# Performance work log

Hardware: AMD Instinct MI355X
Metric: run time of the kernel (lower is better)

## Reference

```python
import jax, jax.numpy as jnp
import numpy as np

LEAK = 0.95
EPS = 1e-4
THRESH = 1.0


def spike_fn(x):
    # forward of SurrogateBPFunction: heaviside(x > 0)
    return (x > 0).astype(x.dtype)


def setup_inputs() -> dict:
    key = jax.random.key(0)
    k1, k2, k3 = jax.random.split(key, 3)
    T, B, D_in, H, C = 20, 512, 4096, 1024, 100
    z = jax.random.normal(k1, (T, B, D_in), dtype=jnp.float32)
    # xavier_uniform with gain=2: bound = 2 * sqrt(6/(fan_in+fan_out))
    b1 = 2.0 * np.sqrt(6.0 / (D_in + H))
    W1 = jax.random.uniform(k2, (H, D_in), dtype=jnp.float32, minval=-b1, maxval=b1)
    b2 = 2.0 * np.sqrt(6.0 / (H + C))
    W2 = jax.random.uniform(k3, (C, H), dtype=jnp.float32, minval=-b2, maxval=b2)
    bn_gamma = jnp.ones((T, H), dtype=jnp.float32)
    return {"z": z, "W1": W1, "bn_gamma": bn_gamma, "W2": W2}


def reference(z, W1, bn_gamma, W2):
    T = z.shape[0]
    B = z.shape[1]
    H = W1.shape[0]
    C = W2.shape[0]

    def step(carry, xs):
        mem1, mem2 = carry
        inp_t, gamma = xs  # inp_t: [B, D_in], gamma: [H]
        h = jnp.einsum('bd,hd->bh', inp_t, W1)  # fc1, no bias
        # BatchNorm1d (training-mode batch stats, affine weight, no bias)
        mean = h.mean(axis=0)
        var = h.var(axis=0)  # biased variance, matches torch BN
        h = gamma * (h - mean) * jax.lax.rsqrt(var + EPS)
        mem1 = LEAK * mem1 + h
        mem_thr = mem1 / THRESH - 1.0
        out = spike_fn(mem_thr)
        rst = jnp.where(mem_thr > 0, THRESH, 0.0).astype(mem1.dtype)
        mem1 = mem1 - rst
        mem2 = mem2 + jnp.einsum('bh,ch->bc', out, W2)
        return (mem1, mem2), None

    mem1_0 = jnp.zeros((B, H), dtype=z.dtype)
    mem2_0 = jnp.zeros((B, C), dtype=z.dtype)
    (mem1, mem2), _ = jax.lax.scan(step, (mem1_0, mem2_0), (z, bn_gamma))
    return mem2 / T
```

## Files before the change

kernel.cpp:

```cpp
#include <hip/hip_runtime.h>
#include <hip/hip_bf16.h>
#include <stdint.h>

typedef _Float16 half8 __attribute__((ext_vector_type(8)));
typedef float f32x4 __attribute__((ext_vector_type(4)));

#define T_STEPS 20
#define B_SZ 512
#define D_IN 4096
#define H_SZ 1024
#define C_SZ 100
#define M_TOT (T_STEPS * B_SZ)
#define BK 32
#define KITERS (D_IN / BK)

__device__ __forceinline__ void gload16(const _Float16* g, _Float16* l) {
  __builtin_amdgcn_global_load_lds(
      (const __attribute__((address_space(1))) void*)g,
      (__attribute__((address_space(3))) void*)l, 16, 0, 0);
}

struct HL {
  half8 h;
  half8 l;
};
__device__ __forceinline__ HL split8(float4 a, float4 b) {
  HL r;
  auto p0 = __builtin_amdgcn_cvt_pkrtz(a.x, a.y);
  auto p1 = __builtin_amdgcn_cvt_pkrtz(a.z, a.w);
  auto p2 = __builtin_amdgcn_cvt_pkrtz(b.x, b.y);
  auto p3 = __builtin_amdgcn_cvt_pkrtz(b.z, b.w);
  r.h[0] = p0.x; r.h[1] = p0.y; r.h[2] = p1.x; r.h[3] = p1.y;
  r.h[4] = p2.x; r.h[5] = p2.y; r.h[6] = p3.x; r.h[7] = p3.y;
  auto q0 = __builtin_amdgcn_cvt_pkrtz(a.x - (float)p0.x, a.y - (float)p0.y);
  auto q1 = __builtin_amdgcn_cvt_pkrtz(a.z - (float)p1.x, a.w - (float)p1.y);
  auto q2 = __builtin_amdgcn_cvt_pkrtz(b.x - (float)p2.x, b.y - (float)p2.y);
  auto q3 = __builtin_amdgcn_cvt_pkrtz(b.z - (float)p3.x, b.w - (float)p3.y);
  r.l[0] = q0.x; r.l[1] = q0.y; r.l[2] = q1.x; r.l[3] = q1.y;
  r.l[4] = q2.x; r.l[5] = q2.y; r.l[6] = q3.x; r.l[7] = q3.y;
  return r;
}

__global__ void k_prep_frag(const float* __restrict__ Z, _Float16* __restrict__ Azh,
                            _Float16* __restrict__ Azl, const float* __restrict__ W1,
                            _Float16* __restrict__ Wfh, _Float16* __restrict__ Wfl) {
  const int ki = blockIdx.x;
  int rt = blockIdx.y;
  const float* src;
  _Float16 *dh, *dl;
  if (rt < 80) {
    src = Z; dh = Azh; dl = Azl;
  } else {
    rt -= 80; src = W1; dh = Wfh; dl = Wfl;
  }
  const int t = threadIdx.x;
#pragma unroll
  for (int p = 0; p < 2; ++p) {
    const int o = t + p * 256;
    const int fb = o >> 6;
    const int j = o & 63;
    const int q = j >> 4;
    const int r = j & 15;
    const float* s = src + (int64_t)(rt * 128 + fb * 16 + r) * D_IN + ki * 32 + q * 8;
    float4 a = *(const float4*)s;
    float4 b = *(const float4*)(s + 4);
    HL hl = split8(a, b);
    const int64_t d = (((int64_t)rt * 128 + ki) * 8 + fb) * 512 + j * 8;
    *(half8*)&dh[d] = hl.h;
    *(half8*)&dl[d] = hl.l;
  }
}

__global__ void k_prep_w2(const float* __restrict__ w2, _Float16* __restrict__ hi,
                          _Float16* __restrict__ lo) {
  int i = blockIdx.x * 256 + threadIdx.x;
  float v = (i < C_SZ * H_SZ) ? w2[i] : 0.0f;
  _Float16 h = (_Float16)v;
  hi[i] = h;
  lo[i] = (_Float16)(v - (float)h);
}

__global__ __launch_bounds__(256) void k_gemm1(
    const _Float16* __restrict__ Ahi, const _Float16* __restrict__ Alo,
    const _Float16* __restrict__ Whi, const _Float16* __restrict__ Wlo,
    float* __restrict__ Hbuf) {
  __shared__ _Float16 sAh[4096];
  __shared__ _Float16 sAl[4096];
  __shared__ _Float16 sWh[4096];
  __shared__ _Float16 sWl[4096];

  const int tid = threadIdx.x;
  const int lane = tid & 63;
  const int w = tid >> 6;

  const int bid = blockIdx.x;
  const int xcd = bid & 7;
  const int q = bid >> 3;
  const int mt = xcd * 10 + (q >> 3);
  const int nt = q & 7;

  const int ls = w * 512 + lane * 8;
  const _Float16* gAh = Ahi + (int64_t)mt * (128 * 4096) + ls;
  const _Float16* gAl = Alo + (int64_t)mt * (128 * 4096) + ls;
  const _Float16* gWh = Whi + (int64_t)nt * (128 * 4096) + ls;
  const _Float16* gWl = Wlo + (int64_t)nt * (128 * 4096) + ls;

  const int wm = (w >> 1) * 64;
  const int wn = (w & 1) * 64;
  const int ra = (wm >> 4) * 512 + lane * 8;
  const int rb = (wn >> 4) * 512 + lane * 8;
  const int fr = lane & 15;
  const int quad = lane >> 4;

  f32x4 acc[4][4] = {};

  for (int ki = 0; ki < KITERS; ++ki) {
    const int64_t so = (int64_t)ki * 4096;
    __syncthreads();
    gload16(gAh + so, &sAh[ls]);
    gload16(gAh + so + 2048, &sAh[ls + 2048]);
    gload16(gAl + so, &sAl[ls]);
    gload16(gAl + so + 2048, &sAl[ls + 2048]);
    gload16(gWh + so, &sWh[ls]);
    gload16(gWh + so + 2048, &sWh[ls + 2048]);
    gload16(gWl + so, &sWl[ls]);
    gload16(gWl + so + 2048, &sWl[ls + 2048]);
    __syncthreads();

    half8 ah[4], al[4], bh[4], bl[4];
#pragma unroll
    for (int i = 0; i < 4; ++i) {
      ah[i] = *(const half8*)&sAh[ra + i * 512];
      al[i] = *(const half8*)&sAl[ra + i * 512];
      bh[i] = *(const half8*)&sWh[rb + i * 512];
      bl[i] = *(const half8*)&sWl[rb + i * 512];
    }
#pragma unroll
    for (int a = 0; a < 4; ++a) {
#pragma unroll
      for (int b = 0; b < 4; ++b) {
        acc[a][b] = __builtin_amdgcn_mfma_f32_16x16x32_f16(ah[a], bh[b], acc[a][b], 0, 0, 0);
        acc[a][b] = __builtin_amdgcn_mfma_f32_16x16x32_f16(ah[a], bl[b], acc[a][b], 0, 0, 0);
        acc[a][b] = __builtin_amdgcn_mfma_f32_16x16x32_f16(al[a], bh[b], acc[a][b], 0, 0, 0);
      }
    }
  }

  const int64_t m0 = (int64_t)mt * 128;
  const int64_t n0 = (int64_t)nt * 128;
#pragma unroll
  for (int a = 0; a < 4; ++a) {
#pragma unroll
    for (int r = 0; r < 4; ++r) {
      const int64_t row = m0 + wm + a * 16 + quad * 4 + r;
      float* dst = Hbuf + row * H_SZ + n0 + wn + fr;
#pragma unroll
      for (int b = 0; b < 4; ++b) dst[b * 16] = acc[a][b][r];
    }
  }
}

__global__ void k_stats(const float* __restrict__ Hbuf, const float* __restrict__ gamma,
                        float* __restrict__ scale, float* __restrict__ shift) {
  const int t = blockIdx.y;
  const int tx = threadIdx.x & 63;
  const int ty = threadIdx.x >> 6;
  const int h = blockIdx.x * 64 + tx;
  const float* p = Hbuf + ((int64_t)t * B_SZ + ty * 128) * H_SZ + h;
  float s = 0.f, s2 = 0.f;
#pragma unroll 8
  for (int i = 0; i < 128; ++i) {
    float v = p[(int64_t)i * H_SZ];
    s += v;
    s2 += v * v;
  }
  __shared__ float ss[4][64];
  __shared__ float sq[4][64];
  ss[ty][tx] = s;
  sq[ty][tx] = s2;
  __syncthreads();
  if (ty == 0) {
    float a = ss[0][tx] + ss[1][tx] + ss[2][tx] + ss[3][tx];
    float b = sq[0][tx] + sq[1][tx] + sq[2][tx] + sq[3][tx];
    const float mean = a * (1.0f / B_SZ);
    const float var = b * (1.0f / B_SZ) - mean * mean;
    const float rs = rsqrtf(var + 1e-4f);
    const float sc = gamma[t * H_SZ + h] * rs;
    scale[t * H_SZ + h] = sc;
    shift[t * H_SZ + h] = -mean * sc;
  }
}

__global__ void k_recur(const float* __restrict__ Hbuf, const float* __restrict__ scale,
                        const float* __restrict__ shift, _Float16* __restrict__ S) {
  const int idx = blockIdx.x * 256 + threadIdx.x;
  const int b = idx >> 10;
  const int h = idx & 1023;
  float mem = 0.f;
  int cnt = 0;
#pragma unroll
  for (int t = 0; t < T_STEPS; ++t) {
    float v = Hbuf[((int64_t)(t * B_SZ + b) << 10) + h];
    v = v * scale[(t << 10) + h] + shift[(t << 10) + h];
    mem = 0.95f * mem + v;
    if (mem - 1.0f > 0.0f) {
      ++cnt;
      mem -= 1.0f;
    }
  }
  S[idx] = (_Float16)cnt;
}

__global__ void k_gemm2(const _Float16* __restrict__ S, const _Float16* __restrict__ W2h,
                        const _Float16* __restrict__ W2l, float* __restrict__ out) {
  const int wid = threadIdx.x >> 6;
  const int lane = threadIdx.x & 63;
  const int m0 = blockIdx.y * 64 + wid * 16;
  const int n0 = blockIdx.x * 16;
  const int fr = lane & 15;
  const int quad = lane >> 4;

  const _Float16* sp = S + (int64_t)(m0 + fr) * H_SZ + quad * 8;
  const _Float16* wph = W2h + (int64_t)(n0 + fr) * H_SZ + quad * 8;
  const _Float16* wpl = W2l + (int64_t)(n0 + fr) * H_SZ + quad * 8;

  f32x4 acc = {0.f, 0.f, 0.f, 0.f};
#pragma unroll 4
  for (int k = 0; k < H_SZ; k += 32) {
    half8 a = *(const half8*)(sp + k);
    half8 bh = *(const half8*)(wph + k);
    half8 bl = *(const half8*)(wpl + k);
    acc = __builtin_amdgcn_mfma_f32_16x16x32_f16(a, bh, acc, 0, 0, 0);
    acc = __builtin_amdgcn_mfma_f32_16x16x32_f16(a, bl, acc, 0, 0, 0);
  }
  const int col = n0 + fr;
  if (col < C_SZ) {
#pragma unroll
    for (int r = 0; r < 4; ++r) {
      const int row = m0 + quad * 4 + r;
      out[row * C_SZ + col] = acc[r] * (1.0f / T_STEPS);
    }
  }
}

extern "C" void kernel_launch(void* const* d_in, const int* in_sizes, int n_in,
                              void* d_out, int out_size, void* d_ws, size_t ws_size,
                              hipStream_t stream) {
  const float* z = (const float*)d_in[0];
  const float* W1 = (const float*)d_in[1];
  const float* gamma = (const float*)d_in[2];
  const float* W2 = (const float*)d_in[3];
  float* out = (float*)d_out;

  char* ws = (char*)d_ws;
  size_t off = 0;
  auto alloc = [&](size_t bytes) -> void* {
    void* p = ws + off;
    off += (bytes + 255) & ~(size_t)255;
    return p;
  };
  _Float16* Azh = (_Float16*)alloc((size_t)M_TOT * D_IN * 2);
  _Float16* Azl = (_Float16*)alloc((size_t)M_TOT * D_IN * 2);
  _Float16* Wfh = (_Float16*)alloc((size_t)H_SZ * D_IN * 2);
  _Float16* Wfl = (_Float16*)alloc((size_t)H_SZ * D_IN * 2);
  float* Hbuf = (float*)alloc((size_t)M_TOT * H_SZ * 4);
  float* scale = (float*)alloc((size_t)T_STEPS * H_SZ * 4);
  float* shift = (float*)alloc((size_t)T_STEPS * H_SZ * 4);
  _Float16* S = (_Float16*)alloc((size_t)B_SZ * H_SZ * 2);
  _Float16* W2h = (_Float16*)alloc((size_t)112 * H_SZ * 2);
  _Float16* W2l = (_Float16*)alloc((size_t)112 * H_SZ * 2);

  dim3 gp(KITERS, 88);
  k_prep_frag<<<gp, 256, 0, stream>>>(z, Azh, Azl, W1, Wfh, Wfl);
  k_prep_w2<<<(112 * H_SZ) / 256, 256, 0, stream>>>(W2, W2h, W2l);

  k_gemm1<<<640, 256, 0, stream>>>(Azh, Azl, Wfh, Wfl, Hbuf);

  dim3 gs(H_SZ / 64, T_STEPS);
  k_stats<<<gs, 256, 0, stream>>>(Hbuf, gamma, scale, shift);

  k_recur<<<(B_SZ * H_SZ) / 256, 256, 0, stream>>>(Hbuf, scale, shift, S);

  dim3 g2(7, 8);
  k_gemm2<<<g2, 256, 0, stream>>>(S, W2h, W2l, out);
}
```

Measured before the change: 548.9 us.

## Fuse BN stats into GEMM epilogue, merge prep kernels with LDS-staged transpose

Removes the separate BatchNorm statistics kernel. The GEMM1 epilogue now reduces per-column sum and sum of squares across lanes and adds them into global buffers with atomics, and the recurrence kernel derives mean and scale on the fly. The Z/W1 fragment prep kernel now reads full contiguous rows and restages them through padded LDS, and the W2 prep is folded into the same launch, cutting launches and improving read coalescing. The trade-offs are atomic contention, a memset, and redundant rsqrt work per element in the recurrence.

```diff
diff --git a/kernel.cpp b/kernel.cpp
--- a/kernel.cpp
+++ b/kernel.cpp
@@ -3,6 +3,7 @@
 #include <stdint.h>
 
 typedef _Float16 half8 __attribute__((ext_vector_type(8)));
+typedef _Float16 half4v __attribute__((ext_vector_type(4)));
 typedef float f32x4 __attribute__((ext_vector_type(4)));
 
 #define T_STEPS 20
@@ -14,38 +15,52 @@
 #define BK 32
 #define KITERS (D_IN / BK)
 
+#define PQ 136
+#define PKI 560
+
 __device__ __forceinline__ void gload16(const _Float16* g, _Float16* l) {
   __builtin_amdgcn_global_load_lds(
       (const __attribute__((address_space(1))) void*)g,
       (__attribute__((address_space(3))) void*)l, 16, 0, 0);
 }
 
-struct HL {
-  half8 h;
-  half8 l;
+struct HL4 {
+  half4v h;
+  half4v l;
 };
-__device__ __forceinline__ HL split8(float4 a, float4 b) {
-  HL r;
+__device__ __forceinline__ HL4 split4(float4 a) {
+  HL4 r;
   auto p0 = __builtin_amdgcn_cvt_pkrtz(a.x, a.y);
   auto p1 = __builtin_amdgcn_cvt_pkrtz(a.z, a.w);
-  auto p2 = __builtin_amdgcn_cvt_pkrtz(b.x, b.y);
-  auto p3 = __builtin_amdgcn_cvt_pkrtz(b.z, b.w);
-  r.h[0] = p0.x; r.h[1] = p0.y; r.h[2] = p1.x; r.h[3] = p1.y;
-  r.h[4] = p2.x; r.h[5] = p2.y; r.h[6] = p3.x; r.h[7] = p3.y;
+  r.h.x = p0.x; r.h.y = p0.y; r.h.z = p1.x; r.h.w = p1.y;
   auto q0 = __builtin_amdgcn_cvt_pkrtz(a.x - (float)p0.x, a.y - (float)p0.y);
   auto q1 = __builtin_amdgcn_cvt_pkrtz(a.z - (float)p1.x, a.w - (float)p1.y);
-  auto q2 = __builtin_amdgcn_cvt_pkrtz(b.x - (float)p2.x, b.y - (float)p2.y);
-  auto q3 = __builtin_amdgcn_cvt_pkrtz(b.z - (float)p3.x, b.w - (float)p3.y);
-  r.l[0] = q0.x; r.l[1] = q0.y; r.l[2] = q1.x; r.l[3] = q1.y;
-  r.l[4] = q2.x; r.l[5] = q2.y; r.l[6] = q3.x; r.l[7] = q3.y;
+  r.l.x = q0.x; r.l.y = q0.y; r.l.z = q1.x; r.l.w = q1.y;
   return r;
 }
 
-__global__ void k_prep_frag(const float* __restrict__ Z, _Float16* __restrict__ Azh,
-                            _Float16* __restrict__ Azl, const float* __restrict__ W1,
-                            _Float16* __restrict__ Wfh, _Float16* __restrict__ Wfl) {
-  const int ki = blockIdx.x;
-  int rt = blockIdx.y;
+__global__ __launch_bounds__(256) void k_prep(
+    const float* __restrict__ Z, _Float16* __restrict__ Azh, _Float16* __restrict__ Azl,
+    const float* __restrict__ W1, _Float16* __restrict__ Wfh, _Float16* __restrict__ Wfl,
+    const float* __restrict__ W2, _Float16* __restrict__ W2h, _Float16* __restrict__ W2l) {
+  const int bid = blockIdx.x;
+  const int tid = threadIdx.x;
+
+  if (bid >= 704) {
+    const int base = (bid - 704) * 1792;
+#pragma unroll
+    for (int i = 0; i < 7; ++i) {
+      const int idx = base + i * 256 + tid;
+      float v = (idx < C_SZ * H_SZ) ? W2[idx] : 0.0f;
+      _Float16 h = (_Float16)v;
+      W2h[idx] = h;
+      W2l[idx] = (_Float16)(v - (float)h);
+    }
+    return;
+  }
+
+  int rt = bid >> 3;
+  const int fb = bid & 7;
   const float* src;
   _Float16 *dh, *dl;
   if (rt < 80) {
@@ -53,37 +68,49 @@
   } else {
     rt -= 80; src = W1; dh = Wfh; dl = Wfl;
   }
-  const int t = threadIdx.x;
-#pragma unroll
-  for (int p = 0; p < 2; ++p) {
-    const int o = t + p * 256;
-    const int fb = o >> 6;
-    const int j = o & 63;
-    const int q = j >> 4;
-    const int r = j & 15;
-    const float* s = src + (int64_t)(rt * 128 + fb * 16 + r) * D_IN + ki * 32 + q * 8;
-    float4 a = *(const float4*)s;
-    float4 b = *(const float4*)(s + 4);
-    HL hl = split8(a, b);
-    const int64_t d = (((int64_t)rt * 128 + ki) * 8 + fb) * 512 + j * 8;
-    *(half8*)&dh[d] = hl.h;
-    *(half8*)&dl[d] = hl.l;
-  }
-}
-
-__global__ void k_prep_w2(const float* __restrict__ w2, _Float16* __restrict__ hi,
-                          _Float16* __restrict__ lo) {
-  int i = blockIdx.x * 256 + threadIdx.x;
-  float v = (i < C_SZ * H_SZ) ? w2[i] : 0.0f;
-  _Float16 h = (_Float16)v;
-  hi[i] = h;
-  lo[i] = (_Float16)(v - (float)h);
+  const float* rowbase = src + (int64_t)(rt * 128 + fb * 16) * D_IN;
+
+  __shared__ _Float16 sH[16 * PKI];
+  __shared__ _Float16 sL[16 * PKI];
+
+  for (int win = 0; win < 8; ++win) {
+#pragma unroll
+    for (int it = 0; it < 8; ++it) {
+      const int idx = it * 256 + tid;
+      const int r = idx >> 7;
+      const int c4 = idx & 127;
+      const int col = c4 * 4;
+      float4 v = *(const float4*)(rowbase + (int64_t)r * D_IN + win * 512 + col);
+      HL4 hl = split4(v);
+      const int ki_l = col >> 5;
+      const int q = (col >> 3) & 3;
+      const int k4 = col & 7;
+      const int d = ki_l * PKI + q * PQ + r * 8 + k4;
+      *(half4v*)&sH[d] = hl.h;
+      *(half4v*)&sL[d] = hl.l;
+    }
+    __syncthreads();
+#pragma unroll
+    for (int it = 0; it < 4; ++it) {
+      const int o = it * 256 + tid;
+      const int ki_l = o >> 6;
+      const int j = o & 63;
+      const int q = j >> 4;
+      const int r = j & 15;
+      const int sidx = ki_l * PKI + q * PQ + r * 8;
+      const int ki = win * 16 + ki_l;
+      const int64_t d = (((int64_t)rt * 128 + ki) * 8 + fb) * 512 + j * 8;
+      *(half8*)&dh[d] = *(const half8*)&sH[sidx];
+      *(half8*)&dl[d] = *(const half8*)&sL[sidx];
+    }
+    __syncthreads();
+  }
 }
 
 __global__ __launch_bounds__(256) void k_gemm1(
     const _Float16* __restrict__ Ahi, const _Float16* __restrict__ Alo,
     const _Float16* __restrict__ Whi, const _Float16* __restrict__ Wlo,
-    float* __restrict__ Hbuf) {
+    float* __restrict__ Hbuf, float* __restrict__ Ssum, float* __restrict__ Ssq) {
   __shared__ _Float16 sAh[4096];
   __shared__ _Float16 sAl[4096];
   __shared__ _Float16 sWh[4096];
@@ -158,41 +185,32 @@
       for (int b = 0; b < 4; ++b) dst[b * 16] = acc[a][b][r];
     }
   }
-}
-
-__global__ void k_stats(const float* __restrict__ Hbuf, const float* __restrict__ gamma,
-                        float* __restrict__ scale, float* __restrict__ shift) {
-  const int t = blockIdx.y;
-  const int tx = threadIdx.x & 63;
-  const int ty = threadIdx.x >> 6;
-  const int h = blockIdx.x * 64 + tx;
-  const float* p = Hbuf + ((int64_t)t * B_SZ + ty * 128) * H_SZ + h;
-  float s = 0.f, s2 = 0.f;
-#pragma unroll 8
-  for (int i = 0; i < 128; ++i) {
-    float v = p[(int64_t)i * H_SZ];
-    s += v;
-    s2 += v * v;
-  }
-  __shared__ float ss[4][64];
-  __shared__ float sq[4][64];
-  ss[ty][tx] = s;
-  sq[ty][tx] = s2;
-  __syncthreads();
-  if (ty == 0) {
-    float a = ss[0][tx] + ss[1][tx] + ss[2][tx] + ss[3][tx];
-    float b = sq[0][tx] + sq[1][tx] + sq[2][tx] + sq[3][tx];
-    const float mean = a * (1.0f / B_SZ);
-    const float var = b * (1.0f / B_SZ) - mean * mean;
-    const float rs = rsqrtf(var + 1e-4f);
-    const float sc = gamma[t * H_SZ + h] * rs;
-    scale[t * H_SZ + h] = sc;
-    shift[t * H_SZ + h] = -mean * sc;
-  }
-}
-
-__global__ void k_recur(const float* __restrict__ Hbuf, const float* __restrict__ scale,
-                        const float* __restrict__ shift, _Float16* __restrict__ S) {
+
+  const int t = mt >> 2;
+#pragma unroll
+  for (int b = 0; b < 4; ++b) {
+    float s = 0.f, s2 = 0.f;
+#pragma unroll
+    for (int a = 0; a < 4; ++a)
+#pragma unroll
+      for (int r = 0; r < 4; ++r) {
+        float v = acc[a][b][r];
+        s += v;
+        s2 += v * v;
+      }
+    s += __shfl_xor(s, 16);  s2 += __shfl_xor(s2, 16);
+    s += __shfl_xor(s, 32);  s2 += __shfl_xor(s2, 32);
+    if (quad == 0) {
+      const int h = (int)n0 + wn + fr + b * 16;
+      atomicAdd(&Ssum[t * H_SZ + h], s);
+      atomicAdd(&Ssq[t * H_SZ + h], s2);
+    }
+  }
+}
+
+__global__ void k_recur(const float* __restrict__ Hbuf, const float* __restrict__ Ssum,
+                        const float* __restrict__ Ssq, const float* __restrict__ gamma,
+                        _Float16* __restrict__ S) {
   const int idx = blockIdx.x * 256 + threadIdx.x;
   const int b = idx >> 10;
   const int h = idx & 1023;
@@ -200,8 +218,11 @@
   int cnt = 0;
 #pragma unroll
   for (int t = 0; t < T_STEPS; ++t) {
+    const float mean = Ssum[(t << 10) + h] * (1.0f / B_SZ);
+    const float var = Ssq[(t << 10) + h] * (1.0f / B_SZ) - mean * mean;
+    const float sc = gamma[(t << 10) + h] * rsqrtf(var + 1e-4f);
     float v = Hbuf[((int64_t)(t * B_SZ + b) << 10) + h];
-    v = v * scale[(t << 10) + h] + shift[(t << 10) + h];
+    v = (v - mean) * sc;
     mem = 0.95f * mem + v;
     if (mem - 1.0f > 0.0f) {
       ++cnt;
@@ -264,22 +285,19 @@
   _Float16* Wfh = (_Float16*)alloc((size_t)H_SZ * D_IN * 2);
   _Float16* Wfl = (_Float16*)alloc((size_t)H_SZ * D_IN * 2);
   float* Hbuf = (float*)alloc((size_t)M_TOT * H_SZ * 4);
-  float* scale = (float*)alloc((size_t)T_STEPS * H_SZ * 4);
-  float* shift = (float*)alloc((size_t)T_STEPS * H_SZ * 4);
+  float* Ssum = (float*)alloc((size_t)T_STEPS * H_SZ * 4);
+  float* Ssq = (float*)alloc((size_t)T_STEPS * H_SZ * 4);
   _Float16* S = (_Float16*)alloc((size_t)B_SZ * H_SZ * 2);
   _Float16* W2h = (_Float16*)alloc((size_t)112 * H_SZ * 2);
   _Float16* W2l = (_Float16*)alloc((size_t)112 * H_SZ * 2);
 
-  dim3 gp(KITERS, 88);
-  k_prep_frag<<<gp, 256, 0, stream>>>(z, Azh, Azl, W1, Wfh, Wfl);
-  k_prep_w2<<<(112 * H_SZ) / 256, 256, 0, stream>>>(W2, W2h, W2l);
-
-  k_gemm1<<<640, 256, 0, stream>>>(Azh, Azl, Wfh, Wfl, Hbuf);
-
-  dim3 gs(H_SZ / 64, T_STEPS);
-  k_stats<<<gs, 256, 0, stream>>>(Hbuf, gamma, scale, shift);
-
-  k_recur<<<(B_SZ * H_SZ) / 256, 256, 0, stream>>>(Hbuf, scale, shift, S);
+  hipMemsetAsync(Ssum, 0, (size_t)2 * T_STEPS * H_SZ * 4, stream);
+
+  k_prep<<<768, 256, 0, stream>>>(z, Azh, Azl, W1, Wfh, Wfl, W2, W2h, W2l);
+
+  k_gemm1<<<640, 256, 0, stream>>>(Azh, Azl, Wfh, Wfl, Hbuf, Ssum, Ssq);
+
+  k_recur<<<(B_SZ * H_SZ) / 256, 256, 0, stream>>>(Hbuf, Ssum, Ssq, gamma, S);
 
   dim3 g2(7, 8);
   k_gemm2<<<g2, 256, 0, stream>>>(S, W2h, W2l, out);
```

Measured after the change: 629.2 us. 1.15x slower.
